# Performance work log

Hardware: AMD Instinct MI355X
Metric: run time of the kernel (lower is better)

## Reference

```python
import jax, jax.numpy as jnp
import numpy as np
import math

N_EMBD = 512
N_BRANCH = 4
BLOCK = 2048
B, T = 2, 2048


def make_rope_tables(dim, max_len):
    inv_freq = 1.0 / (10000.0 ** (np.arange(0, dim, 2, dtype=np.float32) / dim))
    t = np.arange(max_len, dtype=np.float32)
    freqs = np.einsum('i,j->ij', t, inv_freq)  # [max_len, dim/2]
    return jnp.asarray(np.cos(freqs)), jnp.asarray(np.sin(freqs))


def apply_rope(xq, cos, sin):
    # xq: [..., T, C]; cos/sin: [T, C/2]
    x1 = xq[..., 0::2]
    x2 = xq[..., 1::2]
    y1 = x1 * cos - x2 * sin
    y2 = x1 * sin + x2 * cos
    return jnp.stack((y1, y2), axis=-1).reshape(xq.shape)


def setup_inputs() -> dict:
    key = jax.random.key(0)
    ks = jax.random.split(key, 6)
    C, NB = N_EMBD, N_BRANCH
    s = 1.0 / math.sqrt(C)
    a = jax.random.normal(ks[0], (B, T, C), jnp.float32)
    x = jax.random.normal(ks[1], (B, T, C), jnp.float32)
    Wq = jax.random.normal(ks[2], (C, C * NB), jnp.float32) * s
    Wk = jax.random.normal(ks[3], (C, C), jnp.float32) * s
    Wv = jax.random.normal(ks[4], (C, C * NB), jnp.float32) * s
    Wo = jax.random.normal(ks[5], (C, C), jnp.float32) * s
    cos, sin = make_rope_tables(C, BLOCK)
    return {"a": a, "x": x, "Wq": Wq, "Wk": Wk, "Wv": Wv, "Wo": Wo,
            "cos": cos, "sin": sin}


def reference(a, x, Wq, Wk, Wv, Wo, cos, sin):
    Bb, Tt, C = x.shape
    NB = Wq.shape[1] // C
    cos_t = cos[:Tt]
    sin_t = sin[:Tt]

    q = (a @ Wq).reshape(Bb, Tt, NB, C).transpose(0, 2, 1, 3)  # [B,NB,T,C]
    v = (a @ Wv).reshape(Bb, Tt, NB, C).transpose(0, 2, 1, 3)  # [B,NB,T,C]
    k = (x @ Wk)[:, None, :, :]                                # [B,1,T,C]

    q = apply_rope(q, cos_t, sin_t)
    k = apply_rope(k, cos_t, sin_t)

    att = jnp.einsum('bntc,bosc->bnts', q, k) / math.sqrt(C)   # [B,NB,T,T]
    causal = jnp.tril(jnp.ones((Tt, Tt), bool))                # [T,T]
    att_m = jnp.where(causal, att, -jnp.inf)

    # softmax over branch axis; mask is identical across branches, so compute
    # on unmasked logits and zero-out masked positions (== nan_to_num of
    # softmax over fully -inf columns)
    soft_probs = jnp.where(causal, jax.nn.softmax(att, axis=1), 0.0)

    max_val = jnp.max(soft_probs, axis=1, keepdims=True)
    hard_mask = jax.lax.stop_gradient((soft_probs == max_val).astype(att.dtype))
    route_mask = jax.lax.stop_gradient(hard_mask - soft_probs) + soft_probs

    att_max = jnp.max(att_m, axis=1)                           # [B,T,T]
    attn_probs = jax.nn.softmax(att_max, axis=-1)              # [B,T,T]

    combined = attn_probs[:, None, :, :] * route_mask          # [B,NB,T,T]
    y = jnp.einsum('bnts,bnsc->btc', combined, v)              # [B,T,C]
    return y @ Wo
```

## Files before the change

kernel.cpp:

```cpp
#include <hip/hip_runtime.h>
#include <math.h>


#define B_ 2
#define T_ 2048
#define C_ 512
#define NB_ 4
#define C2_ 1024

typedef unsigned short u16;
typedef unsigned char u8;
using short8 = __attribute__((ext_vector_type(8))) short;
using bf16x8 = __attribute__((ext_vector_type(8))) __bf16;
using f32x4  = __attribute__((ext_vector_type(4))) float;

__device__ __forceinline__ float bf2f(u16 u) {
  union { unsigned int i; float f; } v; v.i = ((unsigned int)u) << 16; return v.f;
}
__device__ __forceinline__ u16 f2bf(float f) {
  union { float f; unsigned int i; } v; v.f = f;
  unsigned int u = v.i;
  return (u16)((u + 0x7fffu + ((u >> 16) & 1u)) >> 16);
}
__device__ __forceinline__ f32x4 mfma16x16x32(short8 a, short8 b, f32x4 c) {
  return __builtin_amdgcn_mfma_f32_16x16x32_bf16(
      __builtin_bit_cast(bf16x8, a), __builtin_bit_cast(bf16x8, b), c, 0, 0, 0);
}
__device__ __forceinline__ void split8(const float* s, uint4& hi, uint4& lo) {
  u16 h[8], l[8];
#pragma unroll
  for (int j = 0; j < 8; ++j) {
    h[j] = f2bf(s[j]);
    l[j] = f2bf(s[j] - bf2f(h[j]));
  }
  hi.x = h[0] | ((unsigned)h[1] << 16); hi.y = h[2] | ((unsigned)h[3] << 16);
  hi.z = h[4] | ((unsigned)h[5] << 16); hi.w = h[6] | ((unsigned)h[7] << 16);
  lo.x = l[0] | ((unsigned)l[1] << 16); lo.y = l[2] | ((unsigned)l[3] << 16);
  lo.z = l[4] | ((unsigned)l[5] << 16); lo.w = l[6] | ((unsigned)l[7] << 16);
}
__device__ __forceinline__ int swz(int row) { return ((row >> 1) & 3) << 3; }

__global__ __launch_bounds__(256) void split_a_k(const float* __restrict__ A,
                                                 u16* __restrict__ Acat) {
  const size_t base = ((size_t)blockIdx.x * 256 + threadIdx.x) << 3;
  const size_t row = base >> 9, col = base & 511;
  float av[8];
  *(float4*)(av) = *(const float4*)(&A[base]);
  *(float4*)(av + 4) = *(const float4*)(&A[base + 4]);
  uint4 hi, lo;
  split8(av, hi, lo);
  *(uint4*)(&Acat[row * C2_ + col]) = hi;
  *(uint4*)(&Acat[row * C2_ + C_ + col]) = lo;
}

template <int HILO>
__global__ __launch_bounds__(256) void splitT_w_k(const float* __restrict__ W,
                                                  u16* __restrict__ WT,
                                                  const int N) {
  __shared__ float tile[64][68];
  const int n0 = blockIdx.x << 6, k0 = blockIdx.y << 6;
  const int tid = threadIdx.x;
  const int rr = tid >> 4, cc = (tid & 15) << 2;
#pragma unroll
  for (int it = 0; it < 4; ++it) {
    const int kr = (it << 4) + rr;
    *(float4*)(&tile[kr][cc]) =
        *(const float4*)(&W[(size_t)(k0 + kr) * N + n0 + cc]);
  }
  __syncthreads();
  const int W2 = HILO ? C2_ : C_;
#pragma unroll
  for (int it = 0; it < 4; ++it) {
    const int nr = (it << 4) + rr;
    const int kc = cc;
    float v[4] = {tile[kc][nr], tile[kc + 1][nr], tile[kc + 2][nr],
                  tile[kc + 3][nr]};
    ushort4 hw, lw;
    hw.x = f2bf(v[0]); hw.y = f2bf(v[1]); hw.z = f2bf(v[2]); hw.w = f2bf(v[3]);
    *(ushort4*)(&WT[(size_t)(n0 + nr) * W2 + k0 + kc]) = hw;
    if (HILO) {
      lw.x = f2bf(v[0] - bf2f(hw.x)); lw.y = f2bf(v[1] - bf2f(hw.y));
      lw.z = f2bf(v[2] - bf2f(hw.z)); lw.w = f2bf(v[3] - bf2f(hw.w));
      *(ushort4*)(&WT[(size_t)(n0 + nr) * W2 + C_ + k0 + kc]) = lw;
    }
  }
}

__global__ __launch_bounds__(256) void gemm_qk_pre(const u16* __restrict__ Acat,
                                                   const u16* __restrict__ WT,
                                                   u16* __restrict__ out,
                                                   const float* __restrict__ cosT,
                                                   const float* __restrict__ sinT) {
  __shared__ __align__(16) u16 Ah[64][32], Al[64][32];
  __shared__ __align__(16) u16 Bh[64][32], Bl[64][32];
  const int tid = threadIdx.x;
  const int wave = tid >> 6, lane = tid & 63;
  const int m0 = blockIdx.y << 6, n0 = blockIdx.x << 6;
  const f32x4 zero = {0.f, 0.f, 0.f, 0.f};
  f32x4 acc[4] = {zero, zero, zero, zero};
  const int srow = tid >> 2, kg = (tid & 3) << 3;
  const int lrow = lane & 15, lk = (lane >> 4) << 3;
  const int wrow = wave << 4;
  const size_t abase = (size_t)(m0 + srow) * C2_ + kg;
  const size_t bbase = (size_t)(n0 + srow) * C2_ + kg;
  for (int kk = 0; kk < C_; kk += 32) {
    __builtin_amdgcn_global_load_lds(
        (const __attribute__((address_space(1))) void*)&Acat[abase + kk],
        (__attribute__((address_space(3))) void*)&Ah[wrow][0], 16, 0, 0);
    __builtin_amdgcn_global_load_lds(
        (const __attribute__((address_space(1))) void*)&Acat[abase + C_ + kk],
        (__attribute__((address_space(3))) void*)&Al[wrow][0], 16, 0, 0);
    __builtin_amdgcn_global_load_lds(
        (const __attribute__((address_space(1))) void*)&WT[bbase + kk],
        (__attribute__((address_space(3))) void*)&Bh[wrow][0], 16, 0, 0);
    __builtin_amdgcn_global_load_lds(
        (const __attribute__((address_space(1))) void*)&WT[bbase + C_ + kk],
        (__attribute__((address_space(3))) void*)&Bl[wrow][0], 16, 0, 0);
    __syncthreads();
    short8 ah = *(const short8*)(&Ah[(wave << 4) + lrow][lk]);
    short8 al = *(const short8*)(&Al[(wave << 4) + lrow][lk]);
#pragma unroll
    for (int ns = 0; ns < 4; ++ns) {
      short8 bh = *(const short8*)(&Bh[(ns << 4) + lrow][lk]);
      short8 bl = *(const short8*)(&Bl[(ns << 4) + lrow][lk]);
      acc[ns] = mfma16x16x32(ah, bh, acc[ns]);
      acc[ns] = mfma16x16x32(al, bh, acc[ns]);
      acc[ns] = mfma16x16x32(ah, bl, acc[ns]);
    }
    __syncthreads();
  }
  const int r0 = m0 + (wave << 4) + ((lane >> 4) << 2);
  const int cb = n0 + (lane & 15);
#pragma unroll
  for (int ns = 0; ns < 4; ++ns) {
#pragma unroll
    for (int r = 0; r < 4; ++r) {
      const int rg = r0 + r;
      const int cg = cb + (ns << 4);
      float v = acc[ns][r];
      float pv = __shfl_xor(v, 1);
      const int t = rg & (T_ - 1);
      const int c = cg & (C_ - 1);
      const int i = c >> 1;
      const float cf = cosT[(t << 8) + i];
      const float sf = sinT[(t << 8) + i];
      float x1 = (lane & 1) ? pv : v;
      float x2 = (lane & 1) ? v : pv;
      float y = (lane & 1) ? (x1 * sf + x2 * cf) : (x1 * cf - x2 * sf);
      y *= 0.044194173824159216f;
      const u16 hi = f2bf(y);
      const u16 lo = f2bf(y - bf2f(hi));
      const int b = rg >> 11, n = cg >> 9;
      const size_t rowoff = ((size_t)((b * NB_ + n) * T_ + t)) * C2_;
      out[rowoff + c] = hi;
      out[rowoff + C_ + c] = lo;
    }
  }
}

__global__ __launch_bounds__(256) void gemm_bb(const u16* __restrict__ Acat,
                                               const u16* __restrict__ WT,
                                               u16* __restrict__ out) {
  __shared__ __align__(16) u16 As[64][32];
  __shared__ __align__(16) u16 Bs[64][32];
  const int tid = threadIdx.x;
  const int wave = tid >> 6, lane = tid & 63;
  const int m0 = blockIdx.y << 6, n0 = blockIdx.x << 6;
  const f32x4 zero = {0.f, 0.f, 0.f, 0.f};
  f32x4 acc[4] = {zero, zero, zero, zero};
  const int srow = tid >> 2, kg = (tid & 3) << 3;
  const int lrow = lane & 15, lk = (lane >> 4) << 3;
  const int wrow = wave << 4;
  const size_t abase = (size_t)(m0 + srow) * C2_ + kg;
  const size_t bbase = (size_t)(n0 + srow) * C_ + kg;
  for (int kk = 0; kk < C_; kk += 32) {
    __builtin_amdgcn_global_load_lds(
        (const __attribute__((address_space(1))) void*)&Acat[abase + kk],
        (__attribute__((address_space(3))) void*)&As[wrow][0], 16, 0, 0);
    __builtin_amdgcn_global_load_lds(
        (const __attribute__((address_space(1))) void*)&WT[bbase + kk],
        (__attribute__((address_space(3))) void*)&Bs[wrow][0], 16, 0, 0);
    __syncthreads();
    short8 af = *(const short8*)(&As[(wave << 4) + lrow][lk]);
#pragma unroll
    for (int ns = 0; ns < 4; ++ns) {
      short8 bf = *(const short8*)(&Bs[(ns << 4) + lrow][lk]);
      acc[ns] = mfma16x16x32(af, bf, acc[ns]);
    }
    __syncthreads();
  }
  const int r0 = m0 + (wave << 4) + ((lane >> 4) << 2);
  const int cb = n0 + (lane & 15);
#pragma unroll
  for (int ns = 0; ns < 4; ++ns) {
#pragma unroll
    for (int r = 0; r < 4; ++r) {
      out[(size_t)(r0 + r) * (NB_ * C_) + cb + (ns << 4)] = f2bf(acc[ns][r]);
    }
  }
}

template <int MODE>
__global__ __launch_bounds__(256) void gemm_qk(const float* __restrict__ A,
                                               const float* __restrict__ W,
                                               u16* __restrict__ out,
                                               const float* __restrict__ cosT,
                                               const float* __restrict__ sinT,
                                               const int N, const int K) {
  __shared__ u16 Ah[64][32], Al[64][32];
  __shared__ u16 Bh[64][32], Bl[64][32];
  const int tid = threadIdx.x;
  const int wave = tid >> 6, lane = tid & 63;
  const int m0 = blockIdx.y << 6, n0 = blockIdx.x << 6;
  const f32x4 zero = {0.f, 0.f, 0.f, 0.f};
  f32x4 acc[4] = {zero, zero, zero, zero};
  const int srow = tid >> 2, koff = ((tid & 3) << 3) ^ swz(tid >> 2);
  const int lrow = lane & 15, lk = ((lane >> 4) << 3) ^ swz(lane & 15);
  for (int kk = 0; kk < K; kk += 32) {
    const int kg = (tid & 3) << 3;
    float av[8];
    *(float4*)(av) = *(const float4*)(&A[(size_t)(m0 + srow) * K + kk + kg]);
    *(float4*)(av + 4) =
        *(const float4*)(&A[(size_t)(m0 + srow) * K + kk + kg + 4]);
    uint4 hi, lo;
    split8(av, hi, lo);
    *(uint4*)(&Ah[srow][koff]) = hi;
    *(uint4*)(&Al[srow][koff]) = lo;
    float wv[8];
#pragma unroll
    for (int j = 0; j < 8; ++j)
      wv[j] = W[(size_t)(kk + kg + j) * N + n0 + srow];
    split8(wv, hi, lo);
    *(uint4*)(&Bh[srow][koff]) = hi;
    *(uint4*)(&Bl[srow][koff]) = lo;
    __syncthreads();
    short8 ah = *(const short8*)(&Ah[(wave << 4) + lrow][lk]);
    short8 al = *(const short8*)(&Al[(wave << 4) + lrow][lk]);
#pragma unroll
    for (int ns = 0; ns < 4; ++ns) {
      short8 bh = *(const short8*)(&Bh[(ns << 4) + lrow][lk]);
      short8 bl = *(const short8*)(&Bl[(ns << 4) + lrow][lk]);
      acc[ns] = mfma16x16x32(ah, bh, acc[ns]);
      acc[ns] = mfma16x16x32(al, bh, acc[ns]);
      acc[ns] = mfma16x16x32(ah, bl, acc[ns]);
    }
    __syncthreads();
  }
  const int r0 = m0 + (wave << 4) + ((lane >> 4) << 2);
  const int cb = n0 + (lane & 15);
#pragma unroll
  for (int ns = 0; ns < 4; ++ns) {
#pragma unroll
    for (int r = 0; r < 4; ++r) {
      const int rg = r0 + r;
      const int cg = cb + (ns << 4);
      float v = acc[ns][r];
      float pv = __shfl_xor(v, 1);
      const int t = rg & (T_ - 1);
      const int c = (MODE == 1) ? (cg & (C_ - 1)) : cg;
      const int i = c >> 1;
      const float cf = cosT[(t << 8) + i];
      const float sf = sinT[(t << 8) + i];
      float x1 = (lane & 1) ? pv : v;
      float x2 = (lane & 1) ? v : pv;
      float y = (lane & 1) ? (x1 * sf + x2 * cf) : (x1 * cf - x2 * sf);
      if (MODE == 1) y *= 0.044194173824159216f;
      const u16 hi = f2bf(y);
      const u16 lo = f2bf(y - bf2f(hi));
      size_t rowoff;
      if (MODE == 1) {
        const int b = rg >> 11, n = cg >> 9;
        rowoff = ((size_t)((b * NB_ + n) * T_ + t)) * C2_;
      } else {
        rowoff = (size_t)rg * C2_;
      }
      out[rowoff + c] = hi;
      out[rowoff + C_ + c] = lo;
    }
  }
}

template <int AF32, int OF32>
__global__ __launch_bounds__(256) void gemm_hi(const void* __restrict__ Ap,
                                               const float* __restrict__ W,
                                               void* __restrict__ outp,
                                               const int N, const int K) {
  __shared__ u16 As[64][32];
  __shared__ u16 Bs[64][32];
  const int tid = threadIdx.x;
  const int wave = tid >> 6, lane = tid & 63;
  const int m0 = blockIdx.y << 6, n0 = blockIdx.x << 6;
  const f32x4 zero = {0.f, 0.f, 0.f, 0.f};
  f32x4 acc[4] = {zero, zero, zero, zero};
  const int srow = tid >> 2, koff = ((tid & 3) << 3) ^ swz(tid >> 2);
  const int lrow = lane & 15, lk = ((lane >> 4) << 3) ^ swz(lane & 15);
  for (int kk = 0; kk < K; kk += 32) {
    const int kg = (tid & 3) << 3;
    if (AF32) {
      const float* A = (const float*)Ap;
      float av[8];
      *(float4*)(av) = *(const float4*)(&A[(size_t)(m0 + srow) * K + kk + kg]);
      *(float4*)(av + 4) =
          *(const float4*)(&A[(size_t)(m0 + srow) * K + kk + kg + 4]);
      uint4 hi;
      hi.x = f2bf(av[0]) | ((unsigned)f2bf(av[1]) << 16);
      hi.y = f2bf(av[2]) | ((unsigned)f2bf(av[3]) << 16);
      hi.z = f2bf(av[4]) | ((unsigned)f2bf(av[5]) << 16);
      hi.w = f2bf(av[6]) | ((unsigned)f2bf(av[7]) << 16);
      *(uint4*)(&As[srow][koff]) = hi;
    } else {
      const u16* A = (const u16*)Ap;
      *(uint4*)(&As[srow][koff]) =
          *(const uint4*)(&A[(size_t)(m0 + srow) * K + kk + kg]);
    }
    uint4 hi;
    {
      float w[8];
#pragma unroll
      for (int j = 0; j < 8; ++j)
        w[j] = W[(size_t)(kk + kg + j) * N + n0 + srow];
      hi.x = f2bf(w[0]) | ((unsigned)f2bf(w[1]) << 16);
      hi.y = f2bf(w[2]) | ((unsigned)f2bf(w[3]) << 16);
      hi.z = f2bf(w[4]) | ((unsigned)f2bf(w[5]) << 16);
      hi.w = f2bf(w[6]) | ((unsigned)f2bf(w[7]) << 16);
    }
    *(uint4*)(&Bs[srow][koff]) = hi;
    __syncthreads();
    short8 af = *(const short8*)(&As[(wave << 4) + lrow][lk]);
#pragma unroll
    for (int ns = 0; ns < 4; ++ns) {
      short8 bf = *(const short8*)(&Bs[(ns << 4) + lrow][lk]);
      acc[ns] = mfma16x16x32(af, bf, acc[ns]);
    }
    __syncthreads();
  }
  const int r0 = m0 + (wave << 4) + ((lane >> 4) << 2);
  const int cb = n0 + (lane & 15);
#pragma unroll
  for (int ns = 0; ns < 4; ++ns) {
#pragma unroll
    for (int r = 0; r < 4; ++r) {
      const size_t idx = (size_t)(r0 + r) * N + cb + (ns << 4);
      if (OF32) ((float*)outp)[idx] = acc[ns][r];
      else ((u16*)outp)[idx] = f2bf(acc[ns][r]);
    }
  }
}

__global__ __launch_bounds__(256) void transpose_v_k(const u16* __restrict__ Vraw,
                                                     u16* __restrict__ VT) {
  const int bid = blockIdx.x;
  const int ct = bid & 7;
  const int ttile = (bid >> 3) & 31;
  const int n = (bid >> 8) & 3;
  const int b = bid >> 10;
  __shared__ u16 tile[64][68];
  const int tid = threadIdx.x;
  const int rr = tid >> 4;
  const int cc = (tid & 15) << 2;
  const int t0 = ttile << 6, c0 = ct << 6;
#pragma unroll
  for (int it = 0; it < 4; ++it) {
    const int r = (it << 4) + rr;
    *(ushort4*)(&tile[r][cc]) = *(const ushort4*)(
        &Vraw[((size_t)((b << 11) + t0 + r)) * (NB_ * C_) + n * C_ + c0 + cc]);
  }
  __syncthreads();
#pragma unroll
  for (int it = 0; it < 4; ++it) {
    const int c = (it << 4) + rr;
    ushort4 w;
    w.x = tile[cc + 0][c]; w.y = tile[cc + 1][c];
    w.z = tile[cc + 2][c]; w.w = tile[cc + 3][c];
    *(ushort4*)(&VT[((size_t)((b * NB_ + n) * C_ + c0 + c)) * T_ + t0 + cc]) = w;
  }
}

__global__ __launch_bounds__(256) void scores_k(const u16* __restrict__ Qcat,
                                                const u16* __restrict__ Kcat,
                                                u16* __restrict__ Mout,
                                                u8* __restrict__ Mask) {
  const int tri = ((blockIdx.x & 7) * 66) + (blockIdx.x >> 3);
  int tt = (int)((sqrtf(8.f * (float)tri + 1.f) - 1.f) * 0.5f);
  while ((tt + 1) * (tt + 2) / 2 <= tri) ++tt;
  while (tt * (tt + 1) / 2 > tri) --tt;
  const int ss = tri - tt * (tt + 1) / 2;
  const int b = blockIdx.y;
  __shared__ __align__(16) u16 Qh[NB_][64][32], Ql[NB_][64][32];
  __shared__ __align__(16) u16 Kh[64][32], Kl[64][32];
  const int tid = threadIdx.x;
  const int wave = tid >> 6, lane = tid & 63;
  const int t0 = tt << 6, s0 = ss << 6;
  const f32x4 zero = {0.f, 0.f, 0.f, 0.f};
  f32x4 acc[NB_][4];
  for (int n = 0; n < NB_; ++n)
    for (int j = 0; j < 4; ++j) acc[n][j] = zero;
  const int srow = tid >> 2, kg = (tid & 3) << 3;
  const int lrow = lane & 15, lk = (lane >> 4) << 3;
  const int wrow = wave << 4;
  const size_t qstride = (size_t)T_ * C2_;
  const size_t qbase = ((size_t)(b * NB_ * T_ + t0 + srow)) * C2_ + kg;
  const size_t kbase = ((size_t)((b << 11) + s0 + srow)) * C2_ + kg;

  for (int kk = 0; kk < C_; kk += 32) {
#pragma unroll
    for (int n = 0; n < NB_; ++n) {
      const size_t qb = qbase + (size_t)n * qstride + kk;
      __builtin_amdgcn_global_load_lds(
          (const __attribute__((address_space(1))) void*)&Qcat[qb],
          (__attribute__((address_space(3))) void*)&Qh[n][wrow][0], 16, 0, 0);
      __builtin_amdgcn_global_load_lds(
          (const __attribute__((address_space(1))) void*)&Qcat[qb + C_],
          (__attribute__((address_space(3))) void*)&Ql[n][wrow][0], 16, 0, 0);
    }
    __builtin_amdgcn_global_load_lds(
        (const __attribute__((address_space(1))) void*)&Kcat[kbase + kk],
        (__attribute__((address_space(3))) void*)&Kh[wrow][0], 16, 0, 0);
    __builtin_amdgcn_global_load_lds(
        (const __attribute__((address_space(1))) void*)&Kcat[kbase + kk + C_],
        (__attribute__((address_space(3))) void*)&Kl[wrow][0], 16, 0, 0);
    __syncthreads();
    short8 qh[NB_], ql[NB_];
#pragma unroll
    for (int n = 0; n < NB_; ++n) {
      qh[n] = *(const short8*)(&Qh[n][wrow + lrow][lk]);
      ql[n] = *(const short8*)(&Ql[n][wrow + lrow][lk]);
    }
#pragma unroll
    for (int ns = 0; ns < 4; ++ns) {
      short8 kh = *(const short8*)(&Kh[(ns << 4) + lrow][lk]);
      short8 kl = *(const short8*)(&Kl[(ns << 4) + lrow][lk]);
#pragma unroll
      for (int n = 0; n < NB_; ++n) {
        acc[n][ns] = mfma16x16x32(qh[n], kh, acc[n][ns]);
        acc[n][ns] = mfma16x16x32(ql[n], kh, acc[n][ns]);
        acc[n][ns] = mfma16x16x32(qh[n], kl, acc[n][ns]);
      }
    }
    __syncthreads();
  }
  const int tb = t0 + (wave << 4) + ((lane >> 4) << 2);
  const int sb = s0 + (lane & 15);
#pragma unroll
  for (int ns = 0; ns < 4; ++ns) {
#pragma unroll
    for (int r = 0; r < 4; ++r) {
      const int t = tb + r, s = sb + (ns << 4);
      float a0 = acc[0][ns][r], a1 = acc[1][ns][r];
      float a2 = acc[2][ns][r], a3 = acc[3][ns][r];
      float m = fmaxf(fmaxf(a0, a1), fmaxf(a2, a3));
      u8 msk = (u8)((a0 == m) | ((a1 == m) << 1) | ((a2 == m) << 2) |
                    ((a3 == m) << 3));
      if (s > t) { m = -__builtin_inff(); msk = 0; }
      const size_t idx = (size_t)b * T_ * T_ + (size_t)t * T_ + s;
      Mout[idx] = f2bf(m);
      Mask[idx] = msk;
    }
  }
}

__global__ __launch_bounds__(256) void rowstats_k(const u16* __restrict__ Mb,
                                                  float* __restrict__ Rm,
                                                  float* __restrict__ Rz) {
  const int r = (blockIdx.x << 2) + (threadIdx.x >> 6);
  const int lane = threadIdx.x & 63;
  const int b = r >> 11, t = r & (T_ - 1);
  const u16* row = Mb + (size_t)b * T_ * T_ + (size_t)t * T_;
  float m = -__builtin_inff();
  for (int s = lane; s <= t; s += 64) m = fmaxf(m, bf2f(row[s]));
#pragma unroll
  for (int off = 32; off; off >>= 1) m = fmaxf(m, __shfl_xor(m, off));
  float z = 0.f;
  for (int s = lane; s <= t; s += 64) z += __expf(bf2f(row[s]) - m);
#pragma unroll
  for (int off = 32; off; off >>= 1) z += __shfl_xor(z, off);
  if (lane == 0) { Rm[r] = m; Rz[r] = 1.f / z; }
}

__global__ __launch_bounds__(512) void pv_k(const u16* __restrict__ Mb,
                                            const float* __restrict__ Rm,
                                            const float* __restrict__ Rz,
                                            const u8* __restrict__ Mask,
                                            const u16* __restrict__ VT,
                                            u16* __restrict__ Y) {
  const int cblk = blockIdx.x, ypair = blockIdx.y, b = blockIdx.z;
  const int c0 = cblk << 6;
  __shared__ u16 Ps[NB_][64][32];
  __shared__ u16 Vs[NB_][64][32];
  const int tid = threadIdx.x;
  const int wave = tid >> 6, lane = tid & 63;
  const int wq = wave & 3, ch = wave >> 2;
  const int row8 = tid >> 3, off4 = (tid & 7) << 2;
  const int scol = off4 ^ swz(row8);
  const int lrow = lane & 15, lk = ((lane >> 4) << 3) ^ swz(lane & 15);
  const f32x4 zero = {0.f, 0.f, 0.f, 0.f};
  const size_t vrow_base[NB_] = {
      ((size_t)((b * NB_ + 0) * C_ + c0 + row8)) * T_,
      ((size_t)((b * NB_ + 1) * C_ + c0 + row8)) * T_,
      ((size_t)((b * NB_ + 2) * C_ + c0 + row8)) * T_,
      ((size_t)((b * NB_ + 3) * C_ + c0 + row8)) * T_};

  for (int half = 0; half < 2; ++half) {
    const int tt = half ? (31 - ypair) : ypair;
    const int t0 = tt << 6;
    const int nchunk = (tt + 1) << 1;
    const int rg = (b << 11) + t0 + row8;
    const size_t pro = (size_t)rg << 11;
    const float rm = Rm[rg], rz = Rz[rg];
    f32x4 acc[2] = {zero, zero};
    uint2 puA, puB; unsigned mkA, mkB; uint2 vvA[NB_], vvB[NB_];

    puA = *(const uint2*)(&Mb[pro + off4]);
    mkA = *(const unsigned*)(&Mask[pro + off4]);
#pragma unroll
    for (int n = 0; n < NB_; ++n)
      vvA[n] = *(const uint2*)(&VT[vrow_base[n] + off4]);
    puB = *(const uint2*)(&Mb[pro + 32 + off4]);
    mkB = *(const unsigned*)(&Mask[pro + 32 + off4]);
#pragma unroll
    for (int n = 0; n < NB_; ++n)
      vvB[n] = *(const uint2*)(&VT[vrow_base[n] + 32 + off4]);

    for (int ck = 0; ck < nchunk; ck += 2) {
      {
        u16 m4[4] = {(u16)puA.x, (u16)(puA.x >> 16), (u16)puA.y,
                     (u16)(puA.y >> 16)};
        u16 p[4];
#pragma unroll
        for (int j = 0; j < 4; ++j)
          p[j] = f2bf(__expf(bf2f(m4[j]) - rm) * rz);
        u8 mk[4] = {(u8)mkA, (u8)(mkA >> 8), (u8)(mkA >> 16), (u8)(mkA >> 24)};
#pragma unroll
        for (int n = 0; n < NB_; ++n) {
          uint2 wv;
          wv.x = (unsigned)(((mk[0] >> n) & 1) ? p[0] : 0) |
                 ((unsigned)(((mk[1] >> n) & 1) ? p[1] : 0) << 16);
          wv.y = (unsigned)(((mk[2] >> n) & 1) ? p[2] : 0) |
                 ((unsigned)(((mk[3] >> n) & 1) ? p[3] : 0) << 16);
          *(uint2*)(&Ps[n][row8][scol]) = wv;
          *(uint2*)(&Vs[n][row8][scol]) = vvA[n];
        }
        if (ck + 2 < nchunk) {
          const int sB = (ck + 2) << 5;
          puA = *(const uint2*)(&Mb[pro + sB + off4]);
          mkA = *(const unsigned*)(&Mask[pro + sB + off4]);
#pragma unroll
          for (int n = 0; n < NB_; ++n)
            vvA[n] = *(const uint2*)(&VT[vrow_base[n] + sB + off4]);
        }
        __syncthreads();
#pragma unroll
        for (int n = 0; n < NB_; ++n) {
          short8 af = *(const short8*)(&Ps[n][(wq << 4) + lrow][lk]);
#pragma unroll
          for (int cs = 0; cs < 2; ++cs) {
            short8 bf =
                *(const short8*)(&Vs[n][(ch << 5) + (cs << 4) + lrow][lk]);
            acc[cs] = mfma16x16x32(af, bf, acc[cs]);
          }
        }
        __syncthreads();
      }
      {
        u16 m4[4] = {(u16)puB.x, (u16)(puB.x >> 16), (u16)puB.y,
                     (u16)(puB.y >> 16)};
        u16 p[4];
#pragma unroll
        for (int j = 0; j < 4; ++j)
          p[j] = f2bf(__expf(bf2f(m4[j]) - rm) * rz);
        u8 mk[4] = {(u8)mkB, (u8)(mkB >> 8), (u8)(mkB >> 16), (u8)(mkB >> 24)};
#pragma unroll
        for (int n = 0; n < NB_; ++n) {
          uint2 wv;
          wv.x = (unsigned)(((mk[0] >> n) & 1) ? p[0] : 0) |
                 ((unsigned)(((mk[1] >> n) & 1) ? p[1] : 0) << 16);
          wv.y = (unsigned)(((mk[2] >> n) & 1) ? p[2] : 0) |
                 ((unsigned)(((mk[3] >> n) & 1) ? p[3] : 0) << 16);
          *(uint2*)(&Ps[n][row8][scol]) = wv;
          *(uint2*)(&Vs[n][row8][scol]) = vvB[n];
        }
        if (ck + 3 < nchunk) {
          const int sB = (ck + 3) << 5;
          puB = *(const uint2*)(&Mb[pro + sB + off4]);
          mkB = *(const unsigned*)(&Mask[pro + sB + off4]);
#pragma unroll
          for (int n = 0; n < NB_; ++n)
            vvB[n] = *(const uint2*)(&VT[vrow_base[n] + sB + off4]);
        }
        __syncthreads();
#pragma unroll
        for (int n = 0; n < NB_; ++n) {
          short8 af = *(const short8*)(&Ps[n][(wq << 4) + lrow][lk]);
#pragma unroll
          for (int cs = 0; cs < 2; ++cs) {
            short8 bf =
                *(const short8*)(&Vs[n][(ch << 5) + (cs << 4) + lrow][lk]);
            acc[cs] = mfma16x16x32(af, bf, acc[cs]);
          }
        }
        __syncthreads();
      }
    }
    const int tb = t0 + (wq << 4) + ((lane >> 4) << 2);
    const int cbs = c0 + (ch << 5) + (lane & 15);
#pragma unroll
    for (int cs = 0; cs < 2; ++cs) {
#pragma unroll
      for (int r = 0; r < 4; ++r) {
        Y[(size_t)((b << 11) + tb + r) * C_ + cbs + (cs << 4)] =
            f2bf(acc[cs][r]);
      }
    }
  }
}

extern "C" void kernel_launch(void* const* d_in, const int* in_sizes, int n_in,
                              void* d_out, int out_size, void* d_ws,
                              size_t ws_size, hipStream_t stream) {
  (void)in_sizes; (void)n_in; (void)out_size; (void)ws_size;
  const float* a    = (const float*)d_in[0];
  const float* x    = (const float*)d_in[1];
  const float* Wq   = (const float*)d_in[2];
  const float* Wk   = (const float*)d_in[3];
  const float* Wv   = (const float*)d_in[4];
  const float* Wo   = (const float*)d_in[5];
  const float* cosT = (const float*)d_in[6];
  const float* sinT = (const float*)d_in[7];

  char* w = (char*)d_ws;
  u16* Qcat   = (u16*)(w + 0);
  u16* Kcat   = (u16*)(w + 33554432);
  u16* Vraw   = (u16*)(w + 41943040);
  u16* VT     = (u16*)(w + 58720256);
  u8*  Mask   = (u8*)(w + 75497472);
  float* Rm   = (float*)(w + 83886080);
  float* Rz   = (float*)(w + 83902464);
  u16* Acat   = (u16*)(w + 83918848);
  u16* WTq    = (u16*)(w + 92307456);
  u16* WTv    = (u16*)(w + 96501760);
  u16* Mb     = Vraw;
  u16* Y      = Qcat;

  const dim3 blk(256);
  split_a_k<<<dim3(1024), blk, 0, stream>>>(a, Acat);
  splitT_w_k<1><<<dim3(32, 8), blk, 0, stream>>>(Wq, WTq, 2048);
  splitT_w_k<0><<<dim3(32, 8), blk, 0, stream>>>(Wv, WTv, 2048);
  gemm_qk_pre<<<dim3(32, 64), blk, 0, stream>>>(Acat, WTq, Qcat, cosT, sinT);
  gemm_qk<2><<<dim3(8, 64), blk, 0, stream>>>(x, Wk, Kcat, cosT, sinT, 512, 512);
  gemm_bb<<<dim3(32, 64), blk, 0, stream>>>(Acat, WTv, Vraw);
  transpose_v_k<<<dim3(2048), blk, 0, stream>>>(Vraw, VT);
  scores_k<<<dim3(528, 2), blk, 0, stream>>>(Qcat, Kcat, Mb, Mask);
  rowstats_k<<<dim3(1024), blk, 0, stream>>>(Mb, Rm, Rz);
  pv_k<<<dim3(8, 16, 2), dim3(512), 0, stream>>>(Mb, Rm, Rz, Mask, VT, Y);
  gemm_hi<0, 1><<<dim3(8, 64), blk, 0, stream>>>(Y, Wo, d_out, 512, 512);
}
```

Baseline: 317.0 us.

## Compute two key tiles per block in scores kernel to reuse Q loads

```diff
diff --git a/kernel.cpp b/kernel.cpp
--- a/kernel.cpp
+++ b/kernel.cpp
@@ -380,27 +380,37 @@
                                                 const u16* __restrict__ Kcat,
                                                 u16* __restrict__ Mout,
                                                 u8* __restrict__ Mask) {
-  const int tri = ((blockIdx.x & 7) * 66) + (blockIdx.x >> 3);
-  int tt = (int)((sqrtf(8.f * (float)tri + 1.f) - 1.f) * 0.5f);
-  while ((tt + 1) * (tt + 2) / 2 <= tri) ++tt;
-  while (tt * (tt + 1) / 2 > tri) --tt;
-  const int ss = tri - tt * (tt + 1) / 2;
+  const int gx = blockIdx.x;
+  const int g = gx & 7, j = gx >> 3;
   const int b = blockIdx.y;
+  const int ttA = g, ttB = 31 - g, ttC = g + 8;
+  const int pA = (ttA >> 1) + 1, pB = (ttB >> 1) + 1, pC = (ttC >> 1) + 1;
+  int tt, sp;
+  if (j < pA)           { tt = ttA; sp = j; }
+  else if (j < pA + pB) { tt = ttB; sp = j - pA; }
+  else if (j < pA + pB + pC) { tt = ttC; sp = j - pA - pB; }
+  else                  { tt = 23 - g; sp = j - pA - pB - pC; }
+  const int t0 = tt << 6;
+  const int s0a = (sp << 1) << 6;
+  const bool hasB = ((sp << 1) + 1) <= tt;
+  const int s0b = s0a + 64;
+
   __shared__ __align__(16) u16 Qh[NB_][64][32], Ql[NB_][64][32];
-  __shared__ __align__(16) u16 Kh[64][32], Kl[64][32];
+  __shared__ __align__(16) u16 K0h[64][32], K0l[64][32];
+  __shared__ __align__(16) u16 K1h[64][32], K1l[64][32];
   const int tid = threadIdx.x;
   const int wave = tid >> 6, lane = tid & 63;
-  const int t0 = tt << 6, s0 = ss << 6;
   const f32x4 zero = {0.f, 0.f, 0.f, 0.f};
-  f32x4 acc[NB_][4];
+  f32x4 accA[NB_][4], accB[NB_][4];
   for (int n = 0; n < NB_; ++n)
-    for (int j = 0; j < 4; ++j) acc[n][j] = zero;
+    for (int q = 0; q < 4; ++q) { accA[n][q] = zero; accB[n][q] = zero; }
   const int srow = tid >> 2, kg = (tid & 3) << 3;
   const int lrow = lane & 15, lk = (lane >> 4) << 3;
   const int wrow = wave << 4;
   const size_t qstride = (size_t)T_ * C2_;
   const size_t qbase = ((size_t)(b * NB_ * T_ + t0 + srow)) * C2_ + kg;
-  const size_t kbase = ((size_t)((b << 11) + s0 + srow)) * C2_ + kg;
+  const size_t k0base = ((size_t)((b << 11) + s0a + srow)) * C2_ + kg;
+  const size_t k1base = ((size_t)((b << 11) + s0b + srow)) * C2_ + kg;
 
   for (int kk = 0; kk < C_; kk += 32) {
 #pragma unroll
@@ -414,11 +424,19 @@
           (__attribute__((address_space(3))) void*)&Ql[n][wrow][0], 16, 0, 0);
     }
     __builtin_amdgcn_global_load_lds(
-        (const __attribute__((address_space(1))) void*)&Kcat[kbase + kk],
-        (__attribute__((address_space(3))) void*)&Kh[wrow][0], 16, 0, 0);
+        (const __attribute__((address_space(1))) void*)&Kcat[k0base + kk],
+        (__attribute__((address_space(3))) void*)&K0h[wrow][0], 16, 0, 0);
     __builtin_amdgcn_global_load_lds(
-        (const __attribute__((address_space(1))) void*)&Kcat[kbase + kk + C_],
-        (__attribute__((address_space(3))) void*)&Kl[wrow][0], 16, 0, 0);
+        (const __attribute__((address_space(1))) void*)&Kcat[k0base + kk + C_],
+        (__attribute__((address_space(3))) void*)&K0l[wrow][0], 16, 0, 0);
+    if (hasB) {
+      __builtin_amdgcn_global_load_lds(
+          (const __attribute__((address_space(1))) void*)&Kcat[k1base + kk],
+          (__attribute__((address_space(3))) void*)&K1h[wrow][0], 16, 0, 0);
+      __builtin_amdgcn_global_load_lds(
+          (const __attribute__((address_space(1))) void*)&Kcat[k1base + kk + C_],
+          (__attribute__((address_space(3))) void*)&K1l[wrow][0], 16, 0, 0);
+    }
     __syncthreads();
     short8 qh[NB_], ql[NB_];
 #pragma unroll
@@ -428,33 +446,60 @@
     }
 #pragma unroll
     for (int ns = 0; ns < 4; ++ns) {
-      short8 kh = *(const short8*)(&Kh[(ns << 4) + lrow][lk]);
-      short8 kl = *(const short8*)(&Kl[(ns << 4) + lrow][lk]);
+      short8 kh = *(const short8*)(&K0h[(ns << 4) + lrow][lk]);
+      short8 kl = *(const short8*)(&K0l[(ns << 4) + lrow][lk]);
 #pragma unroll
       for (int n = 0; n < NB_; ++n) {
-        acc[n][ns] = mfma16x16x32(qh[n], kh, acc[n][ns]);
-        acc[n][ns] = mfma16x16x32(ql[n], kh, acc[n][ns]);
-        acc[n][ns] = mfma16x16x32(qh[n], kl, acc[n][ns]);
+        accA[n][ns] = mfma16x16x32(qh[n], kh, accA[n][ns]);
+        accA[n][ns] = mfma16x16x32(ql[n], kh, accA[n][ns]);
+        accA[n][ns] = mfma16x16x32(qh[n], kl, accA[n][ns]);
       }
     }
+    if (hasB) {
+#pragma unroll
+      for (int ns = 0; ns < 4; ++ns) {
+        short8 kh = *(const short8*)(&K1h[(ns << 4) + lrow][lk]);
+        short8 kl = *(const short8*)(&K1l[(ns << 4) + lrow][lk]);
+#pragma unroll
+        for (int n = 0; n < NB_; ++n) {
+          accB[n][ns] = mfma16x16x32(qh[n], kh, accB[n][ns]);
+          accB[n][ns] = mfma16x16x32(ql[n], kh, accB[n][ns]);
+          accB[n][ns] = mfma16x16x32(qh[n], kl, accB[n][ns]);
+        }
+      }
+    }
     __syncthreads();
   }
   const int tb = t0 + (wave << 4) + ((lane >> 4) << 2);
-  const int sb = s0 + (lane & 15);
 #pragma unroll
   for (int ns = 0; ns < 4; ++ns) {
 #pragma unroll
     for (int r = 0; r < 4; ++r) {
-      const int t = tb + r, s = sb + (ns << 4);
-      float a0 = acc[0][ns][r], a1 = acc[1][ns][r];
-      float a2 = acc[2][ns][r], a3 = acc[3][ns][r];
-      float m = fmaxf(fmaxf(a0, a1), fmaxf(a2, a3));
-      u8 msk = (u8)((a0 == m) | ((a1 == m) << 1) | ((a2 == m) << 2) |
-                    ((a3 == m) << 3));
-      if (s > t) { m = -__builtin_inff(); msk = 0; }
-      const size_t idx = (size_t)b * T_ * T_ + (size_t)t * T_ + s;
-      Mout[idx] = f2bf(m);
-      Mask[idx] = msk;
+      const int t = tb + r;
+      {
+        const int s = s0a + (lane & 15) + (ns << 4);
+        float a0 = accA[0][ns][r], a1 = accA[1][ns][r];
+        float a2 = accA[2][ns][r], a3 = accA[3][ns][r];
+        float m = fmaxf(fmaxf(a0, a1), fmaxf(a2, a3));
+        u8 msk = (u8)((a0 == m) | ((a1 == m) << 1) | ((a2 == m) << 2) |
+                      ((a3 == m) << 3));
+        if (s > t) { m = -__builtin_inff(); msk = 0; }
+        const size_t idx = (size_t)b * T_ * T_ + (size_t)t * T_ + s;
+        Mout[idx] = f2bf(m);
+        Mask[idx] = msk;
+      }
+      if (hasB) {
+        const int s = s0b + (lane & 15) + (ns << 4);
+        float a0 = accB[0][ns][r], a1 = accB[1][ns][r];
+        float a2 = accB[2][ns][r], a3 = accB[3][ns][r];
+        float m = fmaxf(fmaxf(a0, a1), fmaxf(a2, a3));
+        u8 msk = (u8)((a0 == m) | ((a1 == m) << 1) | ((a2 == m) << 2) |
+                      ((a3 == m) << 3));
+        if (s > t) { m = -__builtin_inff(); msk = 0; }
+        const size_t idx = (size_t)b * T_ * T_ + (size_t)t * T_ + s;
+        Mout[idx] = f2bf(m);
+        Mask[idx] = msk;
+      }
     }
   }
 }
@@ -649,7 +694,7 @@
   gemm_qk<2><<<dim3(8, 64), blk, 0, stream>>>(x, Wk, Kcat, cosT, sinT, 512, 512);
   gemm_bb<<<dim3(32, 64), blk, 0, stream>>>(Acat, WTv, Vraw);
   transpose_v_k<<<dim3(2048), blk, 0, stream>>>(Vraw, VT);
-  scores_k<<<dim3(528, 2), blk, 0, stream>>>(Qcat, Kcat, Mb, Mask);
+  scores_k<<<dim3(272, 2), blk, 0, stream>>>(Qcat, Kcat, Mb, Mask);
   rowstats_k<<<dim3(1024), blk, 0, stream>>>(Mb, Rm, Rz);
   pv_k<<<dim3(8, 16, 2), dim3(512), 0, stream>>>(Mb, Rm, Rz, Mask, VT, Y);
   gemm_hi<0, 1><<<dim3(8, 64), blk, 0, stream>>>(Y, Wo, d_out, 512, 512);
```

Result: slower. 344.1 us (+8.6%).
